# Kernel optimization log

Measured on AMD Instinct MI355X. Metric: run time of the kernel, lower is better.

Reference implementation:

```python
import jax, jax.numpy as jnp
import numpy as np

NUM_FIELDS = 10
VOCAB_PER_FIELD = 100000
EMBED_DIM = 16
BATCH = 16384


def setup_inputs() -> dict:
    key = jax.random.key(0)
    k1, k2 = jax.random.split(key)
    x = jax.random.randint(k1, (BATCH, NUM_FIELDS), 0, VOCAB_PER_FIELD, dtype=jnp.int64)
    # One embedding table per field, each over the full (summed) vocab,
    # stacked: [F, sum(field_dims), D]
    emb = jax.random.normal(
        k2, (NUM_FIELDS, NUM_FIELDS * VOCAB_PER_FIELD, EMBED_DIM), dtype=jnp.float32
    ) * 0.01
    return {"x": x, "emb": emb}


def reference(x, emb):
    # offsets = cumulative field_dims prefix (all fields have VOCAB_PER_FIELD here)
    offsets = jnp.arange(NUM_FIELDS, dtype=x.dtype) * VOCAB_PER_FIELD  # [F]
    xo = x + offsets[None, :]  # [B, F]
    # xs[i] = emb[i][xo]  ->  gathered[i, b, f, d] = emb[i, xo[b, f], d]
    gathered = emb[:, xo]  # [F, B, F, D]
    ii, jj = jnp.triu_indices(NUM_FIELDS, k=1)  # P = F*(F-1)/2 pairs, i < j
    # pair p=(i,j): xs[j][:, i] * xs[i][:, j]
    ix = gathered[jj, :, ii, :] * gathered[ii, :, jj, :]  # [P, B, D]
    return jnp.transpose(ix, (1, 0, 2))  # [B, P, D]
```

## Files before the change

kernel.cpp:

```cpp
#include <hip/hip_runtime.h>

#define NUM_FIELDS 10
#define VOCAB 100000
#define EMBED_DIM 16
#define BATCH 16384
#define NPAIRS 45
#define ITEMS_PER_THREAD 4

typedef float v4f __attribute__((ext_vector_type(4)));

__device__ __constant__ unsigned short PAIR_IJ[NPAIRS] = {
    0x0100, 0x0200, 0x0300, 0x0400, 0x0500, 0x0600, 0x0700, 0x0800, 0x0900,
    0x0201, 0x0301, 0x0401, 0x0501, 0x0601, 0x0701, 0x0801, 0x0901,
    0x0302, 0x0402, 0x0502, 0x0602, 0x0702, 0x0802, 0x0902,
    0x0403, 0x0503, 0x0603, 0x0703, 0x0803, 0x0903,
    0x0504, 0x0604, 0x0704, 0x0804, 0x0904,
    0x0605, 0x0705, 0x0805, 0x0905,
    0x0706, 0x0806, 0x0906,
    0x0807, 0x0907,
    0x0908
};

__global__ __launch_bounds__(256) void ffm_pair_kernel(
        const int* __restrict__ x,
        const float* __restrict__ emb,
        float* __restrict__ out) {
    const int total  = BATCH * NPAIRS * 4;
    const int stride = total / ITEMS_PER_THREAD;
    const int tid0   = blockIdx.x * blockDim.x + threadIdx.x;
    if (tid0 >= stride) return;

    v4f a[ITEMS_PER_THREAD];
    v4f c[ITEMS_PER_THREAD];

    #pragma unroll
    for (int k = 0; k < ITEMS_PER_THREAD; ++k) {
        const int tid = tid0 + k * stride;
        const int d4 = tid & 3;
        const int bp = tid >> 2;
        const int p  = bp % NPAIRS;
        const int b  = bp / NPAIRS;

        const unsigned int ij = PAIR_IJ[p];
        const int i = (int)(ij & 0xff);
        const int j = (int)(ij >> 8);

        const int xi = x[b * NUM_FIELDS + i] + i * VOCAB;
        const int xj = x[b * NUM_FIELDS + j] + j * VOCAB;

        const size_t rowA = ((size_t)j * (NUM_FIELDS * VOCAB) + (size_t)xi) * EMBED_DIM;
        const size_t rowB = ((size_t)i * (NUM_FIELDS * VOCAB) + (size_t)xj) * EMBED_DIM;

        a[k] = *(const v4f*)(emb + rowA + (size_t)d4 * 4);
        c[k] = *(const v4f*)(emb + rowB + (size_t)d4 * 4);
    }

    #pragma unroll
    for (int k = 0; k < ITEMS_PER_THREAD; ++k) {
        const int tid = tid0 + k * stride;
        const v4f r = a[k] * c[k];
        __builtin_nontemporal_store(r, (v4f*)out + tid);
    }
}

extern "C" void kernel_launch(void* const* d_in, const int* in_sizes, int n_in,
                              void* d_out, int out_size, void* d_ws, size_t ws_size,
                              hipStream_t stream) {
    const int*   x   = (const int*)d_in[0];
    const float* emb = (const float*)d_in[1];
    float*       out = (float*)d_out;

    const int total  = BATCH * NPAIRS * 4;
    const int nthr   = total / ITEMS_PER_THREAD;
    const int block  = 256;
    const int grid   = (nthr + block - 1) / block;

    ffm_pair_kernel<<<grid, block, 0, stream>>>(x, emb, out);
}
```

Baseline: 724.9 us.

## Bucket-sort indices per field so embedding gathers read rows in sorted order

Adds a counting sort of each field's indices (histogram, scan, atomic scatter into workspace) and then runs two passes per pair. The first pass writes one gathered operand to the output, and the second gathers the partner operand in sorted index order and multiplies it in place. The aim is locality in the random gathers from the 640 MB embedding table, since sorted indices let neighbouring threads hit nearby rows in cache. In exchange it adds several small kernels and atomics, and the output is written twice and read once in scattered order. The original single-pass kernel remains as a fallback when the workspace is too small.

```diff
diff --git a/kernel.cpp b/kernel.cpp
--- a/kernel.cpp
+++ b/kernel.cpp
@@ -5,9 +5,122 @@
 #define EMBED_DIM 16
 #define BATCH 16384
 #define NPAIRS 45
-#define ITEMS_PER_THREAD 4
+#define NITEMS (BATCH * NUM_FIELDS)
+#define KBKT 1024
+#define IPT 4
 
 typedef float v4f __attribute__((ext_vector_type(4)));
+
+__device__ __constant__ unsigned char PI[NPAIRS] = {
+    0,0,0,0,0,0,0,0,0, 1,1,1,1,1,1,1,1, 2,2,2,2,2,2,2,
+    3,3,3,3,3,3, 4,4,4,4,4, 5,5,5,5, 6,6,6, 7,7, 8};
+__device__ __constant__ unsigned char PJ[NPAIRS] = {
+    1,2,3,4,5,6,7,8,9, 2,3,4,5,6,7,8,9, 3,4,5,6,7,8,9,
+    4,5,6,7,8,9, 5,6,7,8,9, 6,7,8,9, 7,8,9, 8,9, 9};
+
+#define WS_WORDS (20 * KBKT + NUM_FIELDS * BATCH)
+
+__global__ __launch_bounds__(256) void k_zero(unsigned int* __restrict__ ws) {
+    int t = blockIdx.x * 256 + threadIdx.x;
+    if (t < 10 * KBKT) ws[t] = 0;
+}
+
+__global__ __launch_bounds__(256) void k_hist(const int* __restrict__ x,
+                                              unsigned int* __restrict__ ws) {
+    int t = blockIdx.x * 256 + threadIdx.x;
+    if (t >= NITEMS) return;
+    int i = t % NUM_FIELDS;
+    unsigned int xv = (unsigned int)x[t];
+    atomicAdd(&ws[i * KBKT + (xv >> 7)], 1u);
+}
+
+__global__ __launch_bounds__(KBKT) void k_scan(unsigned int* __restrict__ ws) {
+    __shared__ unsigned int s[KBKT];
+    const int c = blockIdx.x;
+    const int k = threadIdx.x;
+    unsigned int h = ws[c * KBKT + k];
+    s[k] = h;
+    __syncthreads();
+    for (int off = 1; off < KBKT; off <<= 1) {
+        unsigned int v = (k >= off) ? s[k - off] : 0u;
+        __syncthreads();
+        s[k] += v;
+        __syncthreads();
+    }
+    ws[10 * KBKT + c * KBKT + k] = s[k] - h;
+}
+
+__global__ __launch_bounds__(256) void k_scatter(const int* __restrict__ x,
+                                                 unsigned int* __restrict__ ws) {
+    int t = blockIdx.x * 256 + threadIdx.x;
+    if (t >= NITEMS) return;
+    int b = t / NUM_FIELDS;
+    int i = t - b * NUM_FIELDS;
+    unsigned int xv = (unsigned int)x[t];
+    unsigned int pos = atomicAdd(&ws[10 * KBKT + i * KBKT + (xv >> 7)], 1u);
+    ws[20 * KBKT + i * BATCH + pos] = (xv << 14) | (unsigned int)b;
+}
+
+__global__ __launch_bounds__(256) void k_passA(const unsigned int* __restrict__ ws,
+                                               const float* __restrict__ emb,
+                                               float* __restrict__ out) {
+    const unsigned int* sorted = ws + 20 * KBKT;
+    int gtid = blockIdx.x * 256 + threadIdx.x;
+    const int d4 = gtid & 3;
+    const int q  = gtid >> 2;
+    const int tb = q & 4095;
+    const int p  = q >> 12;
+    if (p >= NPAIRS) return;
+    const int i = PI[p], j = PJ[p];
+
+    v4f r[IPT];
+    unsigned int bb[IPT];
+    #pragma unroll
+    for (int k = 0; k < IPT; ++k) {
+        const int t = tb + k * 4096;
+        const unsigned int v = sorted[i * BATCH + t];
+        bb[k] = v & 16383u;
+        const unsigned int xv = v >> 14;
+        const size_t row = ((size_t)j * (NUM_FIELDS * VOCAB)
+                          + (size_t)i * VOCAB + xv) * EMBED_DIM;
+        r[k] = *(const v4f*)(emb + row + (size_t)d4 * 4);
+    }
+    #pragma unroll
+    for (int k = 0; k < IPT; ++k) {
+        *((v4f*)out + (size_t)(bb[k] * NPAIRS + p) * 4 + d4) = r[k];
+    }
+}
+
+__global__ __launch_bounds__(256) void k_passB(const unsigned int* __restrict__ ws,
+                                               const float* __restrict__ emb,
+                                               float* __restrict__ out) {
+    const unsigned int* sorted = ws + 20 * KBKT;
+    int gtid = blockIdx.x * 256 + threadIdx.x;
+    const int d4 = gtid & 3;
+    const int q  = gtid >> 2;
+    const int tb = q & 4095;
+    const int p  = q >> 12;
+    if (p >= NPAIRS) return;
+    const int i = PI[p], j = PJ[p];
+
+    v4f r[IPT];
+    unsigned int bb[IPT];
+    #pragma unroll
+    for (int k = 0; k < IPT; ++k) {
+        const int t = tb + k * 4096;
+        const unsigned int v = sorted[j * BATCH + t];
+        bb[k] = v & 16383u;
+        const unsigned int xv = v >> 14;
+        const size_t row = ((size_t)i * (NUM_FIELDS * VOCAB)
+                          + (size_t)j * VOCAB + xv) * EMBED_DIM;
+        r[k] = *(const v4f*)(emb + row + (size_t)d4 * 4);
+    }
+    #pragma unroll
+    for (int k = 0; k < IPT; ++k) {
+        v4f* op = (v4f*)out + (size_t)(bb[k] * NPAIRS + p) * 4 + d4;
+        *op = *op * r[k];
+    }
+}
 
 __device__ __constant__ unsigned short PAIR_IJ[NPAIRS] = {
     0x0100, 0x0200, 0x0300, 0x0400, 0x0500, 0x0600, 0x0700, 0x0800, 0x0900,
@@ -26,40 +139,31 @@
         const float* __restrict__ emb,
         float* __restrict__ out) {
     const int total  = BATCH * NPAIRS * 4;
-    const int stride = total / ITEMS_PER_THREAD;
+    const int stride = total / 4;
     const int tid0   = blockIdx.x * blockDim.x + threadIdx.x;
     if (tid0 >= stride) return;
-
-    v4f a[ITEMS_PER_THREAD];
-    v4f c[ITEMS_PER_THREAD];
-
+    v4f a[4], c[4];
     #pragma unroll
-    for (int k = 0; k < ITEMS_PER_THREAD; ++k) {
+    for (int k = 0; k < 4; ++k) {
         const int tid = tid0 + k * stride;
         const int d4 = tid & 3;
         const int bp = tid >> 2;
         const int p  = bp % NPAIRS;
         const int b  = bp / NPAIRS;
-
         const unsigned int ij = PAIR_IJ[p];
         const int i = (int)(ij & 0xff);
         const int j = (int)(ij >> 8);
-
         const int xi = x[b * NUM_FIELDS + i] + i * VOCAB;
         const int xj = x[b * NUM_FIELDS + j] + j * VOCAB;
-
         const size_t rowA = ((size_t)j * (NUM_FIELDS * VOCAB) + (size_t)xi) * EMBED_DIM;
         const size_t rowB = ((size_t)i * (NUM_FIELDS * VOCAB) + (size_t)xj) * EMBED_DIM;
-
         a[k] = *(const v4f*)(emb + rowA + (size_t)d4 * 4);
         c[k] = *(const v4f*)(emb + rowB + (size_t)d4 * 4);
     }
-
     #pragma unroll
-    for (int k = 0; k < ITEMS_PER_THREAD; ++k) {
+    for (int k = 0; k < 4; ++k) {
         const int tid = tid0 + k * stride;
-        const v4f r = a[k] * c[k];
-        __builtin_nontemporal_store(r, (v4f*)out + tid);
+        __builtin_nontemporal_store(a[k] * c[k], (v4f*)out + tid);
     }
 }
 
@@ -70,10 +174,20 @@
     const float* emb = (const float*)d_in[1];
     float*       out = (float*)d_out;
 
-    const int total  = BATCH * NPAIRS * 4;
-    const int nthr   = total / ITEMS_PER_THREAD;
-    const int block  = 256;
-    const int grid   = (nthr + block - 1) / block;
+    if (ws_size < (size_t)WS_WORDS * 4) {
+        const int nthr = BATCH * NPAIRS;
+        ffm_pair_kernel<<<(nthr + 255) / 256, 256, 0, stream>>>(x, emb, out);
+        return;
+    }
 
-    ffm_pair_kernel<<<grid, block, 0, stream>>>(x, emb, out);
+    unsigned int* ws = (unsigned int*)d_ws;
+
+    k_zero   <<<(10 * KBKT + 255) / 256, 256, 0, stream>>>(ws);
+    k_hist   <<<(NITEMS + 255) / 256,     256, 0, stream>>>(x, ws);
+    k_scan   <<<NUM_FIELDS, KBKT,              0, stream>>>(ws);
+    k_scatter<<<(NITEMS + 255) / 256,     256, 0, stream>>>(x, ws);
+
+    const int gthreads = NPAIRS * 4096 * 4;
+    k_passA<<<(gthreads + 255) / 256, 256, 0, stream>>>(ws, emb, out);
+    k_passB<<<(gthreads + 255) / 256, 256, 0, stream>>>(ws, emb, out);
 }
```

After: 775.8 us. 7.0% more time.
